# Performance work log

Measured on AMD Instinct MI355X. Metric: run time of the kernel, lower is better.

The kernel has to match this reference:

```python
import jax, jax.numpy as jnp
import numpy as np

D_MODEL = 1024
NUM_HEADS = 16
HEAD_DIM = D_MODEL // NUM_HEADS


def setup_inputs() -> dict:
    key = jax.random.key(0)
    ks = jax.random.split(key, 5)
    B, S = 4, 2048
    scale = 0.02
    return {
        "x": jax.random.normal(ks[0], (B, S, D_MODEL), dtype=jnp.float32),
        "q_proj_weight": jax.random.normal(ks[1], (D_MODEL, D_MODEL), dtype=jnp.float32) * scale,
        "k_proj_weight": jax.random.normal(ks[2], (D_MODEL, D_MODEL), dtype=jnp.float32) * scale,
        "v_proj_weight": jax.random.normal(ks[3], (D_MODEL, D_MODEL), dtype=jnp.float32) * scale,
        "o_proj_weight": jax.random.normal(ks[4], (D_MODEL, D_MODEL), dtype=jnp.float32) * scale,
    }


def reference(x, q_proj_weight, k_proj_weight, v_proj_weight, o_proj_weight):
    B, S, _ = x.shape
    H, Dh = NUM_HEADS, HEAD_DIM

    def proj(w):  # [B,S,d_model] x [d_k,d_in] -> [B,H,S,Dh]
        p = jnp.einsum('bsd,kd->bsk', x, w)
        return p.reshape(B, S, H, Dh).transpose(0, 2, 1, 3)

    q = proj(q_proj_weight)
    k = proj(k_proj_weight)
    v = proj(v_proj_weight)

    scores = jnp.einsum('bhqd,bhkd->bhqk', q, k) / jnp.sqrt(jnp.asarray(Dh, dtype=x.dtype))
    causal = jnp.tril(jnp.ones((S, S), dtype=bool))  # [S,S]
    scores = jnp.where(causal, scores, -jnp.inf)
    attn = jax.nn.softmax(scores, axis=-1)
    out = jnp.einsum('bhqk,bhkd->bhqd', attn, v)  # [B,H,S,Dh]
    out = out.transpose(0, 2, 1, 3).reshape(B, S, D_MODEL)
    return jnp.einsum('bsv,mv->bsm', out, o_proj_weight)
```

## Files before the change

### kernel.cpp

```cpp
#include <hip/hip_runtime.h>
#include <cstdint>
#include <cstddef>

#define NH 16
#define DH 64
#define SEQ 2048
#define DM 1024

typedef __attribute__((ext_vector_type(8))) short short8;
typedef __attribute__((ext_vector_type(4))) float f32x4;

__device__ __forceinline__ unsigned short f2bf(float f) {
  unsigned u = __builtin_bit_cast(unsigned, f);
  u += 0x7fffu + ((u >> 16) & 1u);
  return (unsigned short)(u >> 16);
}

__device__ __forceinline__ void gld_lds16(const void* g, void* l) {
  __builtin_amdgcn_global_load_lds((const __attribute__((address_space(1))) void*)g,
                                   (__attribute__((address_space(3))) void*)l,
                                   16, 0, 0);
}

__global__ __launch_bounds__(256) void cast_all_kernel(const float* __restrict__ x,
                                                       const float* __restrict__ wq,
                                                       const float* __restrict__ wk,
                                                       const float* __restrict__ wv,
                                                       const float* __restrict__ wo,
                                                       unsigned short* __restrict__ xb,
                                                       unsigned short* __restrict__ wqkvb,
                                                       unsigned short* __restrict__ wob) {
  const int bid = blockIdx.x;
  const float* in;
  unsigned short* out;
  int i;
  if (bid < 8192) {
    in = x; out = xb; i = bid * 256 + threadIdx.x;
  } else {
    const int w = (bid - 8192) >> 10;
    i = ((bid - 8192) & 1023) * 256 + threadIdx.x;
    in = (w == 0) ? wq : (w == 1) ? wk : (w == 2) ? wv : wo;
    out = (w < 3) ? (wqkvb + (size_t)w * 1048576) : wob;
  }
  const float4 v = ((const float4*)in)[i];
  ushort4 o;
  o.x = f2bf(v.x); o.y = f2bf(v.y); o.z = f2bf(v.z); o.w = f2bf(v.w);
  ((ushort4*)out)[i] = o;
}

__global__ __launch_bounds__(256, 4) void gemm_qkv(const unsigned short* __restrict__ A,
                                                   const unsigned short* __restrict__ W,
                                                   unsigned short* __restrict__ qb,
                                                   unsigned short* __restrict__ kb,
                                                   unsigned short* __restrict__ vtb) {
  __shared__ __align__(16) unsigned short As[128 * 32];
  __shared__ __align__(16) unsigned short Bs[128 * 32];
  const int t = threadIdx.x;
  const int lane = t & 63;
  const int wave = t >> 6;
  const int quad = lane >> 4;
  const int l16 = lane & 15;
  const int wm = (wave >> 1) * 64;
  const int wn = (wave & 1) * 64;
  const int bm = blockIdx.y * 128;
  const int bn = blockIdx.x * 128;
  const int sel = bn >> 10;
  const int bnl = bn & 1023;

  f32x4 acc[4][4];
#pragma unroll
  for (int i = 0; i < 4; ++i)
#pragma unroll
    for (int j = 0; j < 4; ++j) acc[i][j] = {0.0f, 0.0f, 0.0f, 0.0f};

  const int srow = t >> 2;
  const int sc = (t & 3) ^ ((srow >> 1) & 3);
  const unsigned short* Ag1 = A + (size_t)(bm + srow) * DM + sc * 8;
  const unsigned short* Ag2 = A + (size_t)(bm + srow + 64) * DM + sc * 8;
  const unsigned short* Bg1 = W + (size_t)(bn + srow) * DM + sc * 8;
  const unsigned short* Bg2 = W + (size_t)(bn + srow + 64) * DM + sc * 8;
  const int swz = (l16 >> 1) & 3;

  for (int k0 = 0; k0 < DM; k0 += 32) {
    __syncthreads();
    gld_lds16(Ag1 + k0, As + t * 8);
    gld_lds16(Ag2 + k0, As + t * 8 + 2048);
    gld_lds16(Bg1 + k0, Bs + t * 8);
    gld_lds16(Bg2 + k0, Bs + t * 8 + 2048);
    __syncthreads();
    short8 af[4], bfr[4];
#pragma unroll
    for (int i = 0; i < 4; ++i)
      af[i] = *(const short8*)(As + (wm + i * 16 + l16) * 32 + ((quad ^ swz) * 8));
#pragma unroll
    for (int j = 0; j < 4; ++j)
      bfr[j] = *(const short8*)(Bs + (wn + j * 16 + l16) * 32 + ((quad ^ swz) * 8));
#pragma unroll
    for (int i = 0; i < 4; ++i)
#pragma unroll
      for (int j = 0; j < 4; ++j)
        acc[i][j] = __builtin_amdgcn_mfma_f32_16x16x32_bf16(af[i], bfr[j], acc[i][j], 0, 0, 0);
  }

#pragma unroll
  for (int i = 0; i < 4; ++i) {
#pragma unroll
    for (int j = 0; j < 4; ++j) {
#pragma unroll
      for (int r = 0; r < 4; ++r) {
        const int m = bm + wm + i * 16 + quad * 4 + r;
        const int n = bnl + wn + j * 16 + l16;
        const float v = acc[i][j][r];
        if (sel == 0) {
          qb[(size_t)m * DM + n] = f2bf(v * 0.125f);
        } else if (sel == 1) {
          kb[(size_t)m * DM + n] = f2bf(v);
        } else {
          const int bb = m >> 11, s = m & 2047;
          const int h = n >> 6, d = n & 63;
          vtb[((size_t)((bb * NH + h) * DH + d)) * SEQ + s] = f2bf(v);
        }
      }
    }
  }
}

__global__ __launch_bounds__(256, 4) void gemm_o(const unsigned short* __restrict__ A,
                                                 const unsigned short* __restrict__ B,
                                                 float* __restrict__ C) {
  __shared__ __align__(16) unsigned short As[128 * 32];
  __shared__ __align__(16) unsigned short Bs[128 * 32];
  const int t = threadIdx.x;
  const int lane = t & 63;
  const int wave = t >> 6;
  const int quad = lane >> 4;
  const int l16 = lane & 15;
  const int wm = (wave >> 1) * 64;
  const int wn = (wave & 1) * 64;
  const int bm = blockIdx.y * 128;
  const int bn = blockIdx.x * 128;

  f32x4 acc[4][4];
#pragma unroll
  for (int i = 0; i < 4; ++i)
#pragma unroll
    for (int j = 0; j < 4; ++j) acc[i][j] = {0.0f, 0.0f, 0.0f, 0.0f};

  const int srow = t >> 2;
  const int sc = (t & 3) ^ ((srow >> 1) & 3);
  const unsigned short* Ag1 = A + (size_t)(bm + srow) * DM + sc * 8;
  const unsigned short* Ag2 = A + (size_t)(bm + srow + 64) * DM + sc * 8;
  const unsigned short* Bg1 = B + (size_t)(bn + srow) * DM + sc * 8;
  const unsigned short* Bg2 = B + (size_t)(bn + srow + 64) * DM + sc * 8;
  const int swz = (l16 >> 1) & 3;

  for (int k0 = 0; k0 < DM; k0 += 32) {
    __syncthreads();
    gld_lds16(Ag1 + k0, As + t * 8);
    gld_lds16(Ag2 + k0, As + t * 8 + 2048);
    gld_lds16(Bg1 + k0, Bs + t * 8);
    gld_lds16(Bg2 + k0, Bs + t * 8 + 2048);
    __syncthreads();
    short8 af[4], bfr[4];
#pragma unroll
    for (int i = 0; i < 4; ++i)
      af[i] = *(const short8*)(As + (wm + i * 16 + l16) * 32 + ((quad ^ swz) * 8));
#pragma unroll
    for (int j = 0; j < 4; ++j)
      bfr[j] = *(const short8*)(Bs + (wn + j * 16 + l16) * 32 + ((quad ^ swz) * 8));
#pragma unroll
    for (int i = 0; i < 4; ++i)
#pragma unroll
      for (int j = 0; j < 4; ++j)
        acc[i][j] = __builtin_amdgcn_mfma_f32_16x16x32_bf16(af[i], bfr[j], acc[i][j], 0, 0, 0);
  }

#pragma unroll
  for (int i = 0; i < 4; ++i)
#pragma unroll
    for (int j = 0; j < 4; ++j)
#pragma unroll
      for (int r = 0; r < 4; ++r) {
        const int m = bm + wm + i * 16 + quad * 4 + r;
        const int n = bn + wn + j * 16 + l16;
        C[(size_t)m * DM + n] = acc[i][j][r];
      }
}

__global__ __launch_bounds__(512) void attn_kernel(const unsigned short* __restrict__ Q,
                                                   const unsigned short* __restrict__ K,
                                                   const unsigned short* __restrict__ Vt,
                                                   unsigned short* __restrict__ O) {
  __shared__ __align__(16) unsigned short Ks[64 * 64];
  __shared__ __align__(16) unsigned short Vs[64 * 64];
  __shared__ __align__(16) unsigned short Ps[8][16 * 72];
  const int t = threadIdx.x;
  const int lane = t & 63;
  const int wave = t >> 6;
  const int quad = lane >> 4;
  const int l16 = lane & 15;
  const int h = blockIdx.y;
  const int b = blockIdx.z;

  const int srow = t >> 3;
  const int sc = (t & 7) ^ (srow & 7);
  const int koff = (b * SEQ + srow) * DM + h * 64 + sc * 8;
  const int voff = ((b * NH + h) * DH + srow) * SEQ + sc * 8;
  unsigned short* Pw = &Ps[wave][0];
  const int swz = l16 & 7;

#pragma unroll 1
  for (int pass = 0; pass < 2; ++pass) {
    const int qt = (pass == 0) ? (int)blockIdx.x : 15 - (int)blockIdx.x;
    const int qtile = qt * 128;
    const int row_lo = qtile + wave * 16;
    const int row_hi = row_lo + 15;

    const unsigned short* Qrow =
        Q + ((size_t)(b * SEQ + row_lo + l16)) * DM + h * 64;
    const short8 qf0 = *(const short8*)(Qrow + quad * 8);
    const short8 qf1 = *(const short8*)(Qrow + 32 + quad * 8);

    f32x4 o_acc[4];
#pragma unroll
    for (int nb = 0; nb < 4; ++nb) o_acc[nb] = {0.0f, 0.0f, 0.0f, 0.0f};
    float l_r[4] = {0.0f, 0.0f, 0.0f, 0.0f};

    const int ktiles = 2 * qt + 2;
    for (int kt = 0; kt < ktiles; ++kt) {
      const int kbase = kt * 64;
      __syncthreads();
      gld_lds16(K + koff + (size_t)kbase * DM, Ks + t * 8);
      gld_lds16(Vt + voff + kbase, Vs + t * 8);
      __syncthreads();

      if (kbase <= row_hi) {
        f32x4 s_acc[4];
#pragma unroll
        for (int nb = 0; nb < 4; ++nb) {
          s_acc[nb] = {0.0f, 0.0f, 0.0f, 0.0f};
          const short8 kf0 = *(const short8*)(Ks + (nb * 16 + l16) * 64 + ((quad ^ swz) * 8));
          const short8 kf1 = *(const short8*)(Ks + (nb * 16 + l16) * 64 + (((4 | quad) ^ swz) * 8));
          s_acc[nb] = __builtin_amdgcn_mfma_f32_16x16x32_bf16(qf0, kf0, s_acc[nb], 0, 0, 0);
          s_acc[nb] = __builtin_amdgcn_mfma_f32_16x16x32_bf16(qf1, kf1, s_acc[nb], 0, 0, 0);
        }

        const bool need_mask = (kbase + 63 > row_lo);
#pragma unroll
        for (int r = 0; r < 4; ++r) {
          const int qr = row_lo + quad * 4 + r;
#pragma unroll
          for (int nb = 0; nb < 4; ++nb) {
            float p = __expf(s_acc[nb][r]);
            if (need_mask) p = ((kbase + nb * 16 + l16) <= qr) ? p : 0.0f;
            l_r[r] += p;
            const unsigned u = __builtin_bit_cast(unsigned, p);
            Pw[(quad * 4 + r) * 72 + nb * 16 + l16] =
                (unsigned short)((u + 0x8000u) >> 16);
          }
        }

        const short8 pf0 = *(const short8*)(Pw + l16 * 72 + quad * 8);
        const short8 pf1 = *(const short8*)(Pw + l16 * 72 + 32 + quad * 8);
#pragma unroll
        for (int nb = 0; nb < 4; ++nb) {
          const short8 vf0 = *(const short8*)(Vs + (nb * 16 + l16) * 64 + ((quad ^ swz) * 8));
          const short8 vf1 = *(const short8*)(Vs + (nb * 16 + l16) * 64 + (((4 | quad) ^ swz) * 8));
          o_acc[nb] = __builtin_amdgcn_mfma_f32_16x16x32_bf16(pf0, vf0, o_acc[nb], 0, 0, 0);
          o_acc[nb] = __builtin_amdgcn_mfma_f32_16x16x32_bf16(pf1, vf1, o_acc[nb], 0, 0, 0);
        }
      }
    }

#pragma unroll
    for (int r = 0; r < 4; ++r) {
      float ls = l_r[r];
      ls += __shfl_xor(ls, 1);
      ls += __shfl_xor(ls, 2);
      ls += __shfl_xor(ls, 4);
      ls += __shfl_xor(ls, 8);
      const float inv_l = 1.0f / ls;
      const int qr = row_lo + quad * 4 + r;
#pragma unroll
      for (int nb = 0; nb < 4; ++nb)
        O[((size_t)(b * SEQ + qr)) * DM + h * 64 + nb * 16 + l16] =
            f2bf(o_acc[nb][r] * inv_l);
    }
  }
}

extern "C" void kernel_launch(void* const* d_in, const int* in_sizes, int n_in,
                              void* d_out, int out_size, void* d_ws, size_t ws_size,
                              hipStream_t stream) {
  const float* x  = (const float*)d_in[0];
  const float* wq = (const float*)d_in[1];
  const float* wk = (const float*)d_in[2];
  const float* wv = (const float*)d_in[3];
  const float* wo = (const float*)d_in[4];

  char* ws = (char*)d_ws;
  unsigned short* xb    = (unsigned short*)(ws);
  unsigned short* wqkvb = (unsigned short*)(ws + 16777216);
  unsigned short* wob   = (unsigned short*)(ws + 23068672);
  unsigned short* qb    = (unsigned short*)(ws + 25165824);
  unsigned short* kb    = (unsigned short*)(ws + 41943040);
  unsigned short* vtb   = (unsigned short*)(ws + 58720256);
  unsigned short* aob   = (unsigned short*)(ws + 75497472);

  cast_all_kernel<<<12288, 256, 0, stream>>>(x, wq, wk, wv, wo, xb, wqkvb, wob);

  gemm_qkv<<<dim3(24, 64), 256, 0, stream>>>(xb, wqkvb, qb, kb, vtb);

  attn_kernel<<<dim3(8, NH, 4), 512, 0, stream>>>(qb, kb, vtb, aob);

  gemm_o<<<dim3(8, 64), 256, 0, stream>>>(aob, wob, (float*)d_out);
}
```

Baseline: 271.8 us.

## Double attention KV tile to 128 and remap GEMM blocks for XCD locality

The attention kernel now stages 128 keys per iteration instead of 64. This halves the number of barrier-separated load phases and doubles the MFMA work done per sync, using wider XOR swizzles for the K and transposed-V shared tiles. The QKV and output GEMMs remap the linear block ID so that each XCD handles a contiguous band of row tiles, which should improve L2 reuse of the A operand. The cost is more shared memory per attention block and more masked wasted work on the diagonal tile at the coarser granularity.

```diff
diff --git a/kernel.cpp b/kernel.cpp
--- a/kernel.cpp
+++ b/kernel.cpp
@@ -62,8 +62,12 @@
   const int l16 = lane & 15;
   const int wm = (wave >> 1) * 64;
   const int wn = (wave & 1) * 64;
-  const int bm = blockIdx.y * 128;
-  const int bn = blockIdx.x * 128;
+
+  const int lid = blockIdx.x + 24 * blockIdx.y;
+  const int xcd = lid & 7;
+  const int idx = lid >> 3;
+  const int bm = (xcd * 8 + idx / 24) * 128;
+  const int bn = (idx % 24) * 128;
   const int sel = bn >> 10;
   const int bnl = bn & 1023;
 
@@ -137,8 +141,12 @@
   const int l16 = lane & 15;
   const int wm = (wave >> 1) * 64;
   const int wn = (wave & 1) * 64;
-  const int bm = blockIdx.y * 128;
-  const int bn = blockIdx.x * 128;
+
+  const int lid = blockIdx.x + 8 * blockIdx.y;
+  const int xcd = lid & 7;
+  const int idx = lid >> 3;
+  const int bm = (xcd * 8 + idx / 8) * 128;
+  const int bn = (idx % 8) * 128;
 
   f32x4 acc[4][4];
 #pragma unroll
@@ -191,9 +199,9 @@
                                                    const unsigned short* __restrict__ K,
                                                    const unsigned short* __restrict__ Vt,
                                                    unsigned short* __restrict__ O) {
-  __shared__ __align__(16) unsigned short Ks[64 * 64];
-  __shared__ __align__(16) unsigned short Vs[64 * 64];
-  __shared__ __align__(16) unsigned short Ps[8][16 * 72];
+  __shared__ __align__(16) unsigned short Ks[128 * 64];
+  __shared__ __align__(16) unsigned short Vs[64 * 128];
+  __shared__ __align__(16) unsigned short Ps[8][16 * 136];
   const int t = threadIdx.x;
   const int lane = t & 63;
   const int wave = t >> 6;
@@ -202,10 +210,14 @@
   const int h = blockIdx.y;
   const int b = blockIdx.z;
 
-  const int srow = t >> 3;
-  const int sc = (t & 7) ^ (srow & 7);
-  const int koff = (b * SEQ + srow) * DM + h * 64 + sc * 8;
-  const int voff = ((b * NH + h) * DH + srow) * SEQ + sc * 8;
+  const int ksr1 = t >> 3;
+  const int ksr2 = (t + 512) >> 3;
+  const int koff1 = (b * SEQ + ksr1) * DM + h * 64 + (((t & 7) ^ (ksr1 & 7)) * 8);
+  const int koff2 = (b * SEQ + ksr2) * DM + h * 64 + (((t & 7) ^ (ksr2 & 7)) * 8);
+  const int vsr1 = t >> 4;
+  const int vsr2 = (t + 512) >> 4;
+  const int voff1 = ((b * NH + h) * DH + vsr1) * SEQ + (((t & 15) ^ (vsr1 & 15)) * 8);
+  const int voff2 = ((b * NH + h) * DH + vsr2) * SEQ + (((t & 15) ^ (vsr2 & 15)) * 8);
   unsigned short* Pw = &Ps[wave][0];
   const int swz = l16 & 7;
 
@@ -226,18 +238,20 @@
     for (int nb = 0; nb < 4; ++nb) o_acc[nb] = {0.0f, 0.0f, 0.0f, 0.0f};
     float l_r[4] = {0.0f, 0.0f, 0.0f, 0.0f};
 
-    const int ktiles = 2 * qt + 2;
+    const int ktiles = qt + 1;
     for (int kt = 0; kt < ktiles; ++kt) {
-      const int kbase = kt * 64;
+      const int kbase = kt * 128;
       __syncthreads();
-      gld_lds16(K + koff + (size_t)kbase * DM, Ks + t * 8);
-      gld_lds16(Vt + voff + kbase, Vs + t * 8);
+      gld_lds16(K + koff1 + (size_t)kbase * DM, Ks + t * 8);
+      gld_lds16(K + koff2 + (size_t)kbase * DM, Ks + (t + 512) * 8);
+      gld_lds16(Vt + voff1 + kbase, Vs + t * 8);
+      gld_lds16(Vt + voff2 + kbase, Vs + (t + 512) * 8);
       __syncthreads();
 
       if (kbase <= row_hi) {
-        f32x4 s_acc[4];
-#pragma unroll
-        for (int nb = 0; nb < 4; ++nb) {
+        f32x4 s_acc[8];
+#pragma unroll
+        for (int nb = 0; nb < 8; ++nb) {
           s_acc[nb] = {0.0f, 0.0f, 0.0f, 0.0f};
           const short8 kf0 = *(const short8*)(Ks + (nb * 16 + l16) * 64 + ((quad ^ swz) * 8));
           const short8 kf1 = *(const short8*)(Ks + (nb * 16 + l16) * 64 + (((4 | quad) ^ swz) * 8));
@@ -245,29 +259,30 @@
           s_acc[nb] = __builtin_amdgcn_mfma_f32_16x16x32_bf16(qf1, kf1, s_acc[nb], 0, 0, 0);
         }
 
-        const bool need_mask = (kbase + 63 > row_lo);
+        const bool need_mask = (kbase + 127 > row_lo);
 #pragma unroll
         for (int r = 0; r < 4; ++r) {
           const int qr = row_lo + quad * 4 + r;
 #pragma unroll
-          for (int nb = 0; nb < 4; ++nb) {
+          for (int nb = 0; nb < 8; ++nb) {
             float p = __expf(s_acc[nb][r]);
             if (need_mask) p = ((kbase + nb * 16 + l16) <= qr) ? p : 0.0f;
             l_r[r] += p;
             const unsigned u = __builtin_bit_cast(unsigned, p);
-            Pw[(quad * 4 + r) * 72 + nb * 16 + l16] =
+            Pw[(quad * 4 + r) * 136 + nb * 16 + l16] =
                 (unsigned short)((u + 0x8000u) >> 16);
           }
         }
 
-        const short8 pf0 = *(const short8*)(Pw + l16 * 72 + quad * 8);
-        const short8 pf1 = *(const short8*)(Pw + l16 * 72 + 32 + quad * 8);
-#pragma unroll
-        for (int nb = 0; nb < 4; ++nb) {
-          const short8 vf0 = *(const short8*)(Vs + (nb * 16 + l16) * 64 + ((quad ^ swz) * 8));
-          const short8 vf1 = *(const short8*)(Vs + (nb * 16 + l16) * 64 + (((4 | quad) ^ swz) * 8));
-          o_acc[nb] = __builtin_amdgcn_mfma_f32_16x16x32_bf16(pf0, vf0, o_acc[nb], 0, 0, 0);
-          o_acc[nb] = __builtin_amdgcn_mfma_f32_16x16x32_bf16(pf1, vf1, o_acc[nb], 0, 0, 0);
+#pragma unroll
+        for (int kk = 0; kk < 4; ++kk) {
+          const short8 pf = *(const short8*)(Pw + l16 * 136 + kk * 32 + quad * 8);
+#pragma unroll
+          for (int nb = 0; nb < 4; ++nb) {
+            const short8 vf = *(const short8*)(Vs + (nb * 16 + l16) * 128 +
+                                               (((kk * 4 + quad) ^ l16) * 8));
+            o_acc[nb] = __builtin_amdgcn_mfma_f32_16x16x32_bf16(pf, vf, o_acc[nb], 0, 0, 0);
+          }
         }
       }
     }
```

Result: no change. 269.9 us (-0.7%).
